# Kernel tuning notes

Hardware: AMD Instinct MI355X
Metric: run time of the kernel (lower is better)

The kernel has to match this reference:

```python
import jax, jax.numpy as jnp
import numpy as np

N = 50000        # nodes
E = 800000       # edges
F_IN = 64        # num_features
H = 64           # hidden
DIM = 2          # pseudo-coordinate dim
K = 4            # kernel_size (num Gaussians)
C = 10           # num_classes
G = 50           # graphs in batch
EPS = 1e-15
BN_EPS = 1e-5
ALPHA = 0.01     # leaky relu slope


def _layer_params(key, in_dim):
    k1, k2, k3, k4, k5 = jax.random.split(key, 5)
    return {
        'g': jax.random.normal(k1, (in_dim, K * H), jnp.float32) * 0.05,
        'mu': jax.random.normal(k2, (K, DIM), jnp.float32) * 0.3,
        'sigma': jax.random.uniform(k3, (K, DIM), jnp.float32, 0.5, 1.5),
        'rw': jax.random.normal(k4, (in_dim, H), jnp.float32) * 0.05,
        'b': jax.random.normal(k5, (H,), jnp.float32) * 0.01,
    }


def setup_inputs() -> dict:
    key = jax.random.key(0)
    ks = jax.random.split(key, 16)
    inp = {
        'x': jax.random.normal(ks[0], (N, F_IN), jnp.float32),
        'edge_index': jax.random.randint(ks[1], (2, E), 0, N, jnp.int64),
        'batch_idx': jnp.sort(jax.random.randint(ks[2], (N,), 0, G, jnp.int64)),
        'edge_attr': jax.random.uniform(ks[3], (E, DIM), jnp.float32),
    }
    in_dims = [F_IN, H, H, H]
    for i in range(4):
        p = _layer_params(ks[4 + i], in_dims[i])
        for name, v in p.items():
            inp[f'{name}{i}'] = v
    inp['w_mlp1'] = jax.random.normal(ks[8], (4 * H, H), jnp.float32) * 0.05
    inp['b_mlp1'] = jnp.zeros((H,), jnp.float32)
    inp['bn_gamma'] = jnp.ones((H,), jnp.float32)
    inp['bn_beta'] = jnp.zeros((H,), jnp.float32)
    inp['w_mlp2'] = jax.random.normal(ks[9], (H, C), jnp.float32) * 0.05
    inp['b_mlp2'] = jnp.zeros((C,), jnp.float32)
    return inp


def _gmm_conv(x, src, dst, e, g, mu, sigma, rw, b):
    # PyG GMMConv (separate_gaussians=False, aggr='mean', root_weight=True)
    xg = (x @ g).reshape(-1, K, H)                         # [N, K, H]
    diff = e[:, None, :] - mu[None, :, :]                  # [E, K, DIM]
    gw = jnp.exp(-0.5 * (diff * diff / (EPS + sigma[None] ** 2)).sum(-1))  # [E, K]
    msg = (xg[src] * gw[:, :, None]).sum(axis=1)           # [E, H]
    agg = jax.ops.segment_sum(msg, dst, num_segments=N)    # [N, H]
    deg = jax.ops.segment_sum(jnp.ones((E,), x.dtype), dst, num_segments=N)
    agg = agg / jnp.clip(deg, 1.0, None)[:, None]          # mean aggregation
    return agg + x @ rw + b


def _layer(x, src, dst, e, g, mu, sigma, rw, b):
    # GMMConvLayer: GMMConv -> LeakyReLU(alpha); dropout is identity in eval
    return jax.nn.leaky_relu(_gmm_conv(x, src, dst, e, g, mu, sigma, rw, b), ALPHA)


def reference(x, edge_index, batch_idx, edge_attr,
              g0, mu0, sigma0, rw0, b0,
              g1, mu1, sigma1, rw1, b1,
              g2, mu2, sigma2, rw2, b2,
              g3, mu3, sigma3, rw3, b3,
              w_mlp1, b_mlp1, bn_gamma, bn_beta, w_mlp2, b_mlp2):
    src, dst = edge_index[0], edge_index[1]
    x0 = _layer(x,  src, dst, edge_attr, g0, mu0, sigma0, rw0, b0)
    x1 = _layer(x0, src, dst, edge_attr, g1, mu1, sigma1, rw1, b1)
    x2 = _layer(x1, src, dst, edge_attr, g2, mu2, sigma2, rw2, b2)
    x3 = x0 + x2
    x4 = _layer(x3, src, dst, edge_attr, g3, mu3, sigma3, rw3, b3)
    h = jnp.concatenate([x4, x1, x2, x3], axis=1)          # [N, 4H]
    pooled = jax.ops.segment_max(h, batch_idx, num_segments=G)  # [G, 4H]
    z = pooled @ w_mlp1 + b_mlp1
    # BatchNorm1d in eval mode with running_mean=0, running_var=1
    z = (z / jnp.sqrt(1.0 + BN_EPS)) * bn_gamma + bn_beta
    z = jax.nn.relu(z)
    return z @ w_mlp2 + b_mlp2                              # [G, C]
```

## Files before the change

### kernel.cpp

```cpp
#include <hip/hip_runtime.h>
#include <hip/hip_bf16.h>

#define NN 50000
#define NE 800000
#define NG 50
#define NSL 16
#define NSCB 196
#define NNP (NSCB * 256)
#define NC8 (NNP * 8)

typedef unsigned short u16;
typedef unsigned int u32;
typedef __attribute__((ext_vector_type(8))) short short8;
typedef __attribute__((ext_vector_type(4))) float float4v;
typedef __attribute__((ext_vector_type(2))) float f32x2;

__device__ __forceinline__ float b2f(u16 u) {
    union { u32 i; float f; } v; v.i = ((u32)u) << 16; return v.f;
}
__device__ __forceinline__ u16 f2b(float f) {
    union { float f; u32 i; } v; v.f = f;
    u32 i = v.i;
    return (u16)((i + 0x7FFFu + ((i >> 16) & 1u)) >> 16);
}
__device__ __forceinline__ float lo16f(u32 u) { union { u32 i; float f; } v; v.i = u << 16; return v.f; }
__device__ __forceinline__ float hi16f(u32 u) { union { u32 i; float f; } v; v.i = u & 0xffff0000u; return v.f; }

struct SgP { const float* mu[4]; const float* sg[4]; };
__global__ void k_init(const int* __restrict__ ei_raw, int* flag,
                       int* cnt8, int* startg, int* endg, SgP S, float* __restrict__ gcoef) {
    __shared__ int cs[256];
    int i = blockIdx.x * blockDim.x + threadIdx.x;
    if (i < NC8) cnt8[i] = 0;
    if (i < NG) { startg[i] = 0x7fffffff; endg[i] = 0; }
    if (blockIdx.x == 0 && threadIdx.x < 64) {
        int t = threadIdx.x;
        int l = (t >> 3) & 3, kd = t & 7;
        if (t < 32) {
            float s = S.sg[l][kd];
            gcoef[t] = -0.5f / (1e-15f + s * s);
        } else {
            gcoef[t] = S.mu[l][kd];
        }
    }
    if (blockIdx.x == 1) {
        int t = threadIdx.x;
        cs[t] = (ei_raw[2 * t + 1] == 0) ? 1 : 0;
        __syncthreads();
        for (int d = 128; d > 0; d >>= 1) {
            if (t < d) cs[t] += cs[t + d];
            __syncthreads();
        }
        if (t == 0) *flag = (cs[0] >= 128) ? 1 : 0;
    }
}

struct WParams { const float* g[4]; const float* rw[4]; };
__global__ void k_cvtprep(const int* __restrict__ ei_raw, const int* __restrict__ batch_raw,
                          const int* __restrict__ flag, int* cnt8, u16* __restrict__ rank,
                          const float* __restrict__ x, u16* __restrict__ xb,
                          WParams P, u16* __restrict__ bsw,
                          int* startg, int* endg) {
    int b = blockIdx.x, t = threadIdx.x;
    if (b < 3125) {
        int e = b * 256 + t;
        int w = *flag;
        int s = w ? ei_raw[2 * e] : ei_raw[e];
        int d = w ? ei_raw[2 * (NE + e)] : ei_raw[NE + e];
        int color = s / 6250;
        rank[e] = (u16)atomicAdd(&cnt8[d * 8 + color], 1);
    } else if (b < 6250) {
        int i = (b - 3125) * 256 + t;
        float4 v = *(const float4*)(x + (size_t)i * 4);
        u32 lo = (u32)f2b(v.x) | ((u32)f2b(v.y) << 16);
        u32 hi = (u32)f2b(v.z) | ((u32)f2b(v.w) << 16);
        uint2 pk; pk.x = lo; pk.y = hi;
        *(uint2*)(xb + (size_t)i * 4) = pk;
    } else if (b < 6570) {
        int id = (b - 6250) * 256 + t;
        if (id < 4 * 20480) {
            int l = id / 20480, r = id % 20480;
            int j = r & 7, lane = (r >> 3) & 63, ctkt = r >> 9;
            int ct = ctkt & 3, kt = ctkt >> 2;
            int k = kt * 32 + (lane >> 4) * 8 + j;
            int n = ct * 16 + (lane & 15);
            float v;
            if (k < 256) v = P.g[l][(k & 63) * 256 + (k >> 6) * 64 + n];
            else         v = P.rw[l][(k - 256) * 64 + n];
            bsw[id] = f2b(v);
        }
    } else {
        int n = (b - 6570) * 256 + t;
        if (n >= NN) return;
        int w = *flag;
        int bb = w ? batch_raw[2 * n] : batch_raw[n];
        if (n == 0) {
            startg[bb] = 0;
        } else {
            int bp = w ? batch_raw[2 * (n - 1)] : batch_raw[n - 1];
            if (bp != bb) { startg[bb] = n; endg[bp] = n; }
        }
        if (n == NN - 1) endg[bb] = NN;
    }
}

__global__ __launch_bounds__(256) void k_scanA(const int* __restrict__ cnt8, int* __restrict__ excl8,
                                               int* __restrict__ bsum) {
    __shared__ int s[256];
    int t = threadIdx.x, b = blockIdx.x;
    int n = b * 256 + t;
    uint4 c0 = *(const uint4*)(cnt8 + (size_t)n * 8);
    uint4 c1 = *(const uint4*)(cnt8 + (size_t)n * 8 + 4);
    int v = c0.x + c0.y + c0.z + c0.w + c1.x + c1.y + c1.z + c1.w;
    s[t] = v; __syncthreads();
    for (int d = 1; d < 256; d <<= 1) {
        int x = s[t];
        int y = (t >= d) ? s[t - d] : 0;
        __syncthreads();
        s[t] = x + y;
        __syncthreads();
    }
    int run = s[t] - v;
    uint4 e0, e1;
    e0.x = run;            e0.y = run + c0.x;
    e0.z = e0.y + c0.y;    e0.w = e0.z + c0.z;
    e1.x = e0.w + c0.w;    e1.y = e1.x + c1.x;
    e1.z = e1.y + c1.y;    e1.w = e1.z + c1.z;
    *(uint4*)(excl8 + (size_t)n * 8) = e0;
    *(uint4*)(excl8 + (size_t)n * 8 + 4) = e1;
    if (t == 255) bsum[b] = s[255];
}

__global__ __launch_bounds__(256) void k_scanBC(const int* __restrict__ excl8,
                                                const int* __restrict__ bsum,
                                                int* __restrict__ off8) {
    __shared__ int s[256];
    int t = threadIdx.x, b = blockIdx.x;
    int v = (t < NSCB) ? bsum[t] : 0;
    s[t] = v; __syncthreads();
    for (int d = 1; d < 256; d <<= 1) {
        int x = s[t];
        int y = (t >= d) ? s[t - d] : 0;
        __syncthreads();
        s[t] = x + y;
        __syncthreads();
    }
    int ebase = (b == 0) ? 0 : s[b - 1];
    int n = b * 256 + t;
    uint4 e0 = *(const uint4*)(excl8 + (size_t)n * 8);
    uint4 e1 = *(const uint4*)(excl8 + (size_t)n * 8 + 4);
    e0.x += ebase; e0.y += ebase; e0.z += ebase; e0.w += ebase;
    e1.x += ebase; e1.y += ebase; e1.z += ebase; e1.w += ebase;
    *(uint4*)(off8 + (size_t)n * 8) = e0;
    *(uint4*)(off8 + (size_t)n * 8 + 4) = e1;
}

__global__ void k_scatter(const int* __restrict__ ei_raw, const int* __restrict__ flag,
                          const int* __restrict__ off8, const u16* __restrict__ rank,
                          const float2* __restrict__ eattr2,
                          uint2* __restrict__ rec8) {
    int e = blockIdx.x * blockDim.x + threadIdx.x;
    if (e >= NE) return;
    int w = *flag;
    int s = w ? ei_raw[2 * e] : ei_raw[e];
    int d = w ? ei_raw[2 * (NE + e)] : ei_raw[NE + e];
    int color = s / 6250;
    int slot = off8[d * 8 + color] + (int)rank[e];
    float2 at = eattr2[e];
    u32 q0 = (u32)(fminf(fmaxf(at.x, 0.f), 1.f) * 65535.f + 0.5f);
    u32 q1 = (u32)(fminf(fmaxf(at.y, 0.f), 1.f) * 65535.f + 0.5f);
    uint2 r; r.x = (u32)s; r.y = q0 | (q1 << 16);
    rec8[slot] = r;
}

__global__ __launch_bounds__(256) void k_wgts(const uint2* __restrict__ rec8,
                                              const float* __restrict__ gcoef,
                                              uint2* __restrict__ agw) {
    int j = blockIdx.x * blockDim.x + threadIdx.x;
    if (j >= NE) return;
    uint2 r = rec8[j];
    float a0 = (float)(r.y & 0xffffu) * (1.0f / 65535.0f);
    float a1 = (float)(r.y >> 16) * (1.0f / 65535.0f);
#pragma unroll
    for (int l = 0; l < 4; l++) {
        u16 wq[4];
#pragma unroll
        for (int k = 0; k < 4; k++) {
            float m0 = gcoef[32 + l * 8 + 2 * k], m1 = gcoef[32 + l * 8 + 2 * k + 1];
            float c0 = gcoef[l * 8 + 2 * k],      c1 = gcoef[l * 8 + 2 * k + 1];
            float d0 = a0 - m0, d1 = a1 - m1;
            float t = d0 * d0 * c0 + d1 * d1 * c1;
            wq[k] = f2b(__expf(t));
        }
        uint2 o;
        o.x = (u32)wq[0] | ((u32)wq[1] << 16);
        o.y = (u32)wq[2] | ((u32)wq[3] << 16);
        agw[(size_t)l * NE + j] = o;
    }
}

#define LDA 328
#define ROWS 32
__global__ __launch_bounds__(512, 8) void k_aggemm(const u16* __restrict__ xin,
                                                   const uint2* __restrict__ rec8,
                                                   const uint2* __restrict__ agw,
                                                   const int* __restrict__ off8,
                                                   const u16* __restrict__ bsw,
                                                   const float* __restrict__ bias,
                                                   u16* __restrict__ xout,
                                                   const u16* __restrict__ xadd,
                                                   u16* __restrict__ x3out) {
    __shared__ u16 As[ROWS * LDA];
    int t = threadIdx.x;
    int rbase = blockIdx.x * ROWS;
    int wave = t >> 6, lane = t & 63;
    int sub = lane >> 4;
    int f = lane & 15;

    if (t < 256) {
        int row = t >> 3, pos = t & 7;
        int grow = rbase + row;
        uint4 v = make_uint4(0, 0, 0, 0);
        if (grow < NN) v = *(const uint4*)(xin + (size_t)grow * 64 + pos * 8);
        *(uint4*)(&As[row * LDA + 256 + pos * 8]) = v;
    }

    {
        int row = (wave << 2) + sub;
        int wid = rbase + row;
        int beg = off8[wid * 8], end = off8[wid * 8 + 8];
        int endm1 = end - 1;
        f32x2 acc[4][2];
#pragma unroll
        for (int k = 0; k < 4; k++) {
            acc[k][0] = (f32x2){0.f, 0.f};
            acc[k][1] = (f32x2){0.f, 0.f};
        }
        int nb = (end - beg + 3) >> 2;
        for (int bt = 0; bt < nb; bt++) {
            int j0 = beg + bt * 4;
            u32 s[4]; uint2 wv[4];
#pragma unroll
            for (int u = 0; u < 4; u++) {
                int j = j0 + u;
                int jc = j < endm1 ? j : endm1;
                bool ok = j < end;
                s[u] = rec8[jc].x;
                uint2 w = agw[jc];
                wv[u].x = ok ? w.x : 0u;
                wv[u].y = ok ? w.y : 0u;
            }
            uint2 xr[4];
#pragma unroll
            for (int u = 0; u < 4; u++)
                xr[u] = *(const uint2*)(xin + (size_t)s[u] * 64 + f * 4);
#pragma unroll
            for (int u = 0; u < 4; u++) {
                f32x2 x01, x23;
                x01.x = lo16f(xr[u].x); x01.y = hi16f(xr[u].x);
                x23.x = lo16f(xr[u].y); x23.y = hi16f(xr[u].y);
                float w0 = lo16f(wv[u].x), w1 = hi16f(wv[u].x);
                float w2 = lo16f(wv[u].y), w3 = hi16f(wv[u].y);
                acc[0][0] += w0 * x01; acc[0][1] += w0 * x23;
                acc[1][0] += w1 * x01; acc[1][1] += w1 * x23;
                acc[2][0] += w2 * x01; acc[2][1] += w2 * x23;
                acc[3][0] += w3 * x01; acc[3][1] += w3 * x23;
            }
        }
        int deg = end - beg;
        float sc = 1.0f / (float)(deg > 1 ? deg : 1);
#pragma unroll
        for (int k = 0; k < 4; k++) {
            u16 o0 = f2b(acc[k][0].x * sc), o1 = f2b(acc[k][0].y * sc);
            u16 o2 = f2b(acc[k][1].x * sc), o3 = f2b(acc[k][1].y * sc);
            uint2 pk;
            pk.x = (u32)o0 | ((u32)o1 << 16);
            pk.y = (u32)o2 | ((u32)o3 << 16);
            *(uint2*)(&As[row * LDA + k * 64 + f * 4]) = pk;
        }
    }
    __syncthreads();

    int lr = lane & 15, lg = lane >> 4;
    int rt = wave & 1;
    int ct = wave >> 1;
    const u16* ar = &As[(rt * 16 + lr) * LDA + lg * 8];
    const uint4* bp = (const uint4*)bsw;
    float4v acc0 = {0.f, 0.f, 0.f, 0.f};
    for (int kt = 0; kt < 10; kt++) {
        short8 a  = *(const short8*)(ar + kt * 32);
        short8 b0 = *(const short8*)(bp + (kt * 4 + ct) * 64 + lane);
        acc0 = __builtin_amdgcn_mfma_f32_16x16x32_bf16(a, b0, acc0, 0, 0, 0);
    }
    {
        int col = ct * 16 + lr;
        float bv = bias[col];
#pragma unroll
        for (int reg = 0; reg < 4; reg++) {
            int grow = rbase + rt * 16 + lg * 4 + reg;
            if (grow < NN) {
                float v = acc0[reg] + bv;
                v = v > 0.f ? v : 0.01f * v;
                xout[(size_t)grow * 64 + col] = f2b(v);
                if (x3out) {
                    float s2 = v + b2f(xadd[(size_t)grow * 64 + col]);
                    x3out[(size_t)grow * 64 + col] = f2b(s2);
                }
            }
        }
    }
}

__global__ __launch_bounds__(256) void k_pool1(const u16* __restrict__ x4, const u16* __restrict__ x1,
                                               const u16* __restrict__ x2, const u16* __restrict__ x3,
                                               const int* __restrict__ startg, const int* __restrict__ endg,
                                               float* __restrict__ partial) {
    int g = blockIdx.x, sl = blockIdx.y;
    int c = threadIdx.x;
    const u16* arr = (c < 64) ? x4 : (c < 128) ? x1 : (c < 192) ? x2 : x3;
    int h = c & 63;
    int s = startg[g], e = endg[g];
    int len = e - s;
    int chunk = (len + NSL - 1) / NSL;
    int s0 = s + sl * chunk;
    int e0 = s0 + chunk; if (e0 > e) e0 = e;
    float m = -3.4e38f;
    for (int n = s0; n < e0; n++) {
        float v = b2f(arr[(size_t)n * 64 + h]);
        m = v > m ? v : m;
    }
    partial[((size_t)g * NSL + sl) * 256 + c] = m;
}

__global__ __launch_bounds__(256) void k_final(const float* __restrict__ partial, const float* __restrict__ w1,
                        const float* __restrict__ b1, const float* __restrict__ gamma,
                        const float* __restrict__ beta, const float* __restrict__ w2,
                        const float* __restrict__ b2v, float* __restrict__ out) {
    __shared__ float pld[256];
    __shared__ float part[256];
    __shared__ float zsh[64];
    int g = blockIdx.x, t = threadIdx.x;
    int h = t & 63, jq = t >> 6;
    {
        float m = -3.4e38f;
#pragma unroll
        for (int sl = 0; sl < NSL; sl++) {
            float v = partial[((size_t)g * NSL + sl) * 256 + t];
            m = v > m ? v : m;
        }
        pld[t] = m;
    }
    __syncthreads();
    float z = 0.f;
    for (int j = jq * 64; j < jq * 64 + 64; j++) z += pld[j] * w1[j * 64 + h];
    part[t] = z;
    __syncthreads();
    if (t < 64) {
        float zz = b1[t] + part[t] + part[64 + t] + part[128 + t] + part[192 + t];
        zz = zz * 0.9999950000374997f * gamma[t] + beta[t];
        zz = zz > 0.f ? zz : 0.f;
        zsh[t] = zz;
    }
    __syncthreads();
    if (t < 10) {
        float o = b2v[t];
        for (int k = 0; k < 64; k++) o += zsh[k] * w2[k * 10 + t];
        out[g * 10 + t] = o;
    }
}

extern "C" void kernel_launch(void* const* d_in, const int* in_sizes, int n_in,
                              void* d_out, int out_size, void* d_ws, size_t ws_size,
                              hipStream_t stream) {
    const float* x_in    = (const float*)d_in[0];
    const int* ei_raw    = (const int*)d_in[1];
    const int* batch_raw = (const int*)d_in[2];
    const float* eattr   = (const float*)d_in[3];

    const float *g_[4], *mu_[4], *sg_[4], *rw_[4], *b_[4];
    for (int i = 0; i < 4; i++) {
        g_[i]  = (const float*)d_in[4 + 5 * i + 0];
        mu_[i] = (const float*)d_in[4 + 5 * i + 1];
        sg_[i] = (const float*)d_in[4 + 5 * i + 2];
        rw_[i] = (const float*)d_in[4 + 5 * i + 3];
        b_[i]  = (const float*)d_in[4 + 5 * i + 4];
    }
    const float* w_mlp1 = (const float*)d_in[24];
    const float* b_mlp1 = (const float*)d_in[25];
    const float* bn_g   = (const float*)d_in[26];
    const float* bn_b   = (const float*)d_in[27];
    const float* w_mlp2 = (const float*)d_in[28];
    const float* b_mlp2 = (const float*)d_in[29];
    float* out = (float*)d_out;

    char* ws = (char*)d_ws;
    size_t o = 0;
    auto take = [&](size_t bytes) { size_t r = o; o += (bytes + 255) & ~(size_t)255; return r; };
    int*    flag     = (int*)(ws + take(4));
    float*  gcoef    = (float*)(ws + take(64 * 4));
    u16*    rank     = (u16*)(ws + take((size_t)NE * 2));
    int*    cnt8     = (int*)(ws + take((size_t)NC8 * 4));
    int*    excl8    = (int*)(ws + take((size_t)NC8 * 4));
    int*    off8     = (int*)(ws + take((size_t)(NC8 + 8) * 4));
    int*    bsum     = (int*)(ws + take((size_t)NSCB * 4));
    uint2*  rec8     = (uint2*)(ws + take((size_t)NE * 8));
    uint2*  agw      = (uint2*)(ws + take((size_t)4 * NE * 8));
    u16*    xb       = (u16*)(ws + take((size_t)NN * 64 * 2));
    u16*    x0       = (u16*)(ws + take((size_t)NN * 64 * 2));
    u16*    x1       = (u16*)(ws + take((size_t)NN * 64 * 2));
    u16*    x2       = (u16*)(ws + take((size_t)NN * 64 * 2));
    u16*    x3       = (u16*)(ws + take((size_t)NN * 64 * 2));
    u16*    x4       = (u16*)(ws + take((size_t)NN * 64 * 2));
    u16*    bsw      = (u16*)(ws + take((size_t)4 * 320 * 64 * 2));
    float*  partial  = (float*)(ws + take((size_t)NG * NSL * 256 * 4));
    int*    startg   = (int*)(ws + take(NG * 4));
    int*    endg     = (int*)(ws + take(NG * 4));
    (void)ws_size; (void)in_sizes; (void)n_in; (void)out_size;

    SgP SP;
    for (int i = 0; i < 4; i++) { SP.mu[i] = mu_[i]; SP.sg[i] = sg_[i]; }
    k_init<<<dim3((NC8 + 255) / 256), dim3(256), 0, stream>>>(ei_raw, flag, cnt8, startg, endg, SP, gcoef);

    WParams WP;
    for (int i = 0; i < 4; i++) { WP.g[i] = g_[i]; WP.rw[i] = rw_[i]; }
    k_cvtprep<<<dim3(6766), dim3(256), 0, stream>>>(
        ei_raw, batch_raw, flag, cnt8, rank, x_in, xb, WP, bsw, startg, endg);

    k_scanA<<<dim3(NSCB), dim3(256), 0, stream>>>(cnt8, excl8, bsum);
    k_scanBC<<<dim3(NSCB), dim3(256), 0, stream>>>(excl8, bsum, off8);
    k_scatter<<<dim3(NE / 256), dim3(256), 0, stream>>>(
        ei_raw, flag, off8, rank, (const float2*)eattr, rec8);
    k_wgts<<<dim3(NE / 256), dim3(256), 0, stream>>>(rec8, gcoef, agw);

    const int agGrid = (NN + ROWS - 1) / ROWS;
    const u16* lin[4]  = {xb, x0, x1, x3};
    u16*       lout[4] = {x0, x1, x2, x4};
    for (int l = 0; l < 4; l++) {
        k_aggemm<<<dim3(agGrid), dim3(512), 0, stream>>>(
            lin[l], rec8, agw + (size_t)l * NE, off8,
            bsw + (size_t)l * 20480, b_[l], lout[l],
            (l == 2) ? x0 : (const u16*)nullptr,
            (l == 2) ? x3 : (u16*)nullptr);
    }

    k_pool1<<<dim3(NG, NSL), dim3(256), 0, stream>>>(x4, x1, x2, x3, startg, endg, partial);
    k_final<<<dim3(NG), dim3(256), 0, stream>>>(partial, w_mlp1, b_mlp1, bn_g, bn_b, w_mlp2, b_mlp2, out);
}
```

Before: 339.6 us.

## Sort nodes by degree bucket to balance per-row aggregation work

Builds a permutation of nodes grouped by in-degree bucket using a block-local histogram plus global atomic counters in the scan kernels, then has the aggregation-GEMM kernel process nodes in that order. Rows handled by the same wavefront get similar edge counts, cutting divergence and tail imbalance in the per-node edge loop. It costs extra indirection loads through the permutation, scattered row reads and writes of node features, and a slightly larger grid that covers padded rows.

```diff
diff --git a/kernel.cpp b/kernel.cpp
--- a/kernel.cpp
+++ b/kernel.cpp
@@ -28,11 +28,14 @@
 
 struct SgP { const float* mu[4]; const float* sg[4]; };
 __global__ void k_init(const int* __restrict__ ei_raw, int* flag,
-                       int* cnt8, int* startg, int* endg, SgP S, float* __restrict__ gcoef) {
+                       int* cnt8, int* startg, int* endg, SgP S, float* __restrict__ gcoef,
+                       int* dcnt) {
     __shared__ int cs[256];
     int i = blockIdx.x * blockDim.x + threadIdx.x;
     if (i < NC8) cnt8[i] = 0;
     if (i < NG) { startg[i] = 0x7fffffff; endg[i] = 0; }
+    if (i < 64 && blockIdx.x == 2) dcnt[threadIdx.x] = 0;
+    if (blockIdx.x == 2 && threadIdx.x < 64) dcnt[threadIdx.x] = 0;
     if (blockIdx.x == 0 && threadIdx.x < 64) {
         int t = threadIdx.x;
         int l = (t >> 3) & 3, kd = t & 7;
@@ -105,13 +108,16 @@
 }
 
 __global__ __launch_bounds__(256) void k_scanA(const int* __restrict__ cnt8, int* __restrict__ excl8,
-                                               int* __restrict__ bsum) {
+                                               int* __restrict__ bsum, int* dcnt, int* __restrict__ pnr) {
     __shared__ int s[256];
+    __shared__ int hcnt[64];
+    __shared__ int hbase[64];
     int t = threadIdx.x, b = blockIdx.x;
     int n = b * 256 + t;
     uint4 c0 = *(const uint4*)(cnt8 + (size_t)n * 8);
     uint4 c1 = *(const uint4*)(cnt8 + (size_t)n * 8 + 4);
     int v = c0.x + c0.y + c0.z + c0.w + c1.x + c1.y + c1.z + c1.w;
+    if (t < 64) hcnt[t] = 0;
     s[t] = v; __syncthreads();
     for (int d = 1; d < 256; d <<= 1) {
         int x = s[t];
@@ -129,15 +135,28 @@
     *(uint4*)(excl8 + (size_t)n * 8) = e0;
     *(uint4*)(excl8 + (size_t)n * 8 + 4) = e1;
     if (t == 255) bsum[b] = s[255];
+    int nb;
+    if (n < NN) { nb = (v + 3) >> 2; if (nb > 62) nb = 62; } else nb = 63;
+    int lrank = atomicAdd(&hcnt[nb], 1);
+    __syncthreads();
+    if (t < 64) hbase[t] = atomicAdd(&dcnt[t], hcnt[t]);
+    __syncthreads();
+    pnr[n] = (nb << 20) | (hbase[nb] + lrank);
 }
 
 __global__ __launch_bounds__(256) void k_scanBC(const int* __restrict__ excl8,
                                                 const int* __restrict__ bsum,
-                                                int* __restrict__ off8) {
+                                                int* __restrict__ off8,
+                                                const int* __restrict__ dcnt,
+                                                const int* __restrict__ pnr,
+                                                int* __restrict__ perm) {
     __shared__ int s[256];
+    __shared__ int dsc[64];
     int t = threadIdx.x, b = blockIdx.x;
     int v = (t < NSCB) ? bsum[t] : 0;
-    s[t] = v; __syncthreads();
+    s[t] = v;
+    if (t < 64) dsc[t] = dcnt[t];
+    __syncthreads();
     for (int d = 1; d < 256; d <<= 1) {
         int x = s[t];
         int y = (t >= d) ? s[t - d] : 0;
@@ -153,6 +172,13 @@
     e1.x += ebase; e1.y += ebase; e1.z += ebase; e1.w += ebase;
     *(uint4*)(off8 + (size_t)n * 8) = e0;
     *(uint4*)(off8 + (size_t)n * 8 + 4) = e1;
+    if (t == 0) {
+        int runb = 0;
+        for (int i = 0; i < 64; i++) { int c = dsc[i]; dsc[i] = runb; runb += c; }
+    }
+    __syncthreads();
+    int pv = pnr[n];
+    perm[dsc[pv >> 20] + (pv & 0xFFFFF)] = n;
 }
 
 __global__ void k_scatter(const int* __restrict__ ei_raw, const int* __restrict__ flag,
@@ -205,6 +231,7 @@
                                                    const uint2* __restrict__ rec8,
                                                    const uint2* __restrict__ agw,
                                                    const int* __restrict__ off8,
+                                                   const int* __restrict__ perm,
                                                    const u16* __restrict__ bsw,
                                                    const float* __restrict__ bias,
                                                    u16* __restrict__ xout,
@@ -219,7 +246,7 @@
 
     if (t < 256) {
         int row = t >> 3, pos = t & 7;
-        int grow = rbase + row;
+        int grow = perm[rbase + row];
         uint4 v = make_uint4(0, 0, 0, 0);
         if (grow < NN) v = *(const uint4*)(xin + (size_t)grow * 64 + pos * 8);
         *(uint4*)(&As[row * LDA + 256 + pos * 8]) = v;
@@ -227,7 +254,7 @@
 
     {
         int row = (wave << 2) + sub;
-        int wid = rbase + row;
+        int wid = perm[rbase + row];
         int beg = off8[wid * 8], end = off8[wid * 8 + 8];
         int endm1 = end - 1;
         f32x2 acc[4][2];
@@ -297,7 +324,7 @@
         float bv = bias[col];
 #pragma unroll
         for (int reg = 0; reg < 4; reg++) {
-            int grow = rbase + rt * 16 + lg * 4 + reg;
+            int grow = perm[rbase + rt * 16 + lg * 4 + reg];
             if (grow < NN) {
                 float v = acc0[reg] + bv;
                 v = v > 0.f ? v : 0.01f * v;
@@ -398,11 +425,14 @@
     auto take = [&](size_t bytes) { size_t r = o; o += (bytes + 255) & ~(size_t)255; return r; };
     int*    flag     = (int*)(ws + take(4));
     float*  gcoef    = (float*)(ws + take(64 * 4));
+    int*    dcnt     = (int*)(ws + take(64 * 4));
     u16*    rank     = (u16*)(ws + take((size_t)NE * 2));
     int*    cnt8     = (int*)(ws + take((size_t)NC8 * 4));
     int*    excl8    = (int*)(ws + take((size_t)NC8 * 4));
     int*    off8     = (int*)(ws + take((size_t)(NC8 + 8) * 4));
     int*    bsum     = (int*)(ws + take((size_t)NSCB * 4));
+    int*    pnr      = (int*)(ws + take((size_t)NNP * 4));
+    int*    perm     = (int*)(ws + take((size_t)NNP * 4));
     uint2*  rec8     = (uint2*)(ws + take((size_t)NE * 8));
     uint2*  agw      = (uint2*)(ws + take((size_t)4 * NE * 8));
     u16*    xb       = (u16*)(ws + take((size_t)NN * 64 * 2));
@@ -419,25 +449,25 @@
 
     SgP SP;
     for (int i = 0; i < 4; i++) { SP.mu[i] = mu_[i]; SP.sg[i] = sg_[i]; }
-    k_init<<<dim3((NC8 + 255) / 256), dim3(256), 0, stream>>>(ei_raw, flag, cnt8, startg, endg, SP, gcoef);
+    k_init<<<dim3((NC8 + 255) / 256), dim3(256), 0, stream>>>(ei_raw, flag, cnt8, startg, endg, SP, gcoef, dcnt);
 
     WParams WP;
     for (int i = 0; i < 4; i++) { WP.g[i] = g_[i]; WP.rw[i] = rw_[i]; }
     k_cvtprep<<<dim3(6766), dim3(256), 0, stream>>>(
         ei_raw, batch_raw, flag, cnt8, rank, x_in, xb, WP, bsw, startg, endg);
 
-    k_scanA<<<dim3(NSCB), dim3(256), 0, stream>>>(cnt8, excl8, bsum);
-    k_scanBC<<<dim3(NSCB), dim3(256), 0, stream>>>(excl8, bsum, off8);
+    k_scanA<<<dim3(NSCB), dim3(256), 0, stream>>>(cnt8, excl8, bsum, dcnt, pnr);
+    k_scanBC<<<dim3(NSCB), dim3(256), 0, stream>>>(excl8, bsum, off8, dcnt, pnr, perm);
     k_scatter<<<dim3(NE / 256), dim3(256), 0, stream>>>(
         ei_raw, flag, off8, rank, (const float2*)eattr, rec8);
     k_wgts<<<dim3(NE / 256), dim3(256), 0, stream>>>(rec8, gcoef, agw);
 
-    const int agGrid = (NN + ROWS - 1) / ROWS;
+    const int agGrid = NNP / ROWS;
     const u16* lin[4]  = {xb, x0, x1, x3};
     u16*       lout[4] = {x0, x1, x2, x4};
     for (int l = 0; l < 4; l++) {
         k_aggemm<<<dim3(agGrid), dim3(512), 0, stream>>>(
-            lin[l], rec8, agw + (size_t)l * NE, off8,
+            lin[l], rec8, agw + (size_t)l * NE, off8, perm,
             bsw + (size_t)l * 20480, b_[l], lout[l],
             (l == 2) ? x0 : (const u16*)nullptr,
             (l == 2) ? x3 : (u16*)nullptr);
```

Result: faster. 328.7 us (-3.2%).
